# Performance work log

Measured on AMD Instinct MI355X. Metric: run time of the kernel, lower is better.

The kernel has to match this reference:

```python
import jax, jax.numpy as jnp
import numpy as np
import math

B, HW, C, HEADS = 32, 784, 384, 8
T = HW + 1            # 785 tokens incl. cls
TP = HW // 4 + 1      # 197 tokens after pooling
FF = 4 * C
EPS = 1e-5


def _ln2d(x, w, b):
    # nn.LayerNorm over last two dims (tokens, channels) with affine params
    mu = x.mean(axis=(-2, -1), keepdims=True)
    var = x.var(axis=(-2, -1), keepdims=True)
    return (x - mu) / jnp.sqrt(var + EPS) * w + b


def setup_inputs() -> dict:
    key = jax.random.key(0)
    ks = jax.random.split(key, 10)
    sc = math.sqrt(2.0 / C)  # kaiming-ish scale
    rn = lambda k, sh, s=1.0: (jax.random.normal(k, sh, jnp.float32) * s)
    return {
        "x": rn(ks[0], (B, HW, C)),
        "cls_token": rn(ks[1], (B, 1, C)),
        "w_ln1": jnp.ones((T, C), jnp.float32),
        "b_ln1": jnp.zeros((T, C), jnp.float32),
        "Wq": rn(ks[2], (C, C), sc),
        "Wk": rn(ks[3], (C, C), sc),
        "Wv": rn(ks[4], (C, C), sc),
        "Wo": rn(ks[5], (C, C), sc),
        "w_ln2": jnp.ones((TP, C), jnp.float32),
        "b_ln2": jnp.zeros((TP, C), jnp.float32),
        "W1": rn(ks[6], (FF, C), sc),
        "W2": rn(ks[7], (C, FF), math.sqrt(2.0 / FF)),
    }


def reference(x, cls_token, w_ln1, b_ln1, Wq, Wk, Wv, Wo, w_ln2, b_ln2, W1, W2):
    d = C // HEADS
    x_in = jnp.concatenate([cls_token, x], axis=1)           # (B,T,C)
    x1 = _ln2d(x_in, w_ln1, b_ln1)
    # MHSA (dropout disabled for determinism)
    q = (x1 @ Wq.T).reshape(B, T, HEADS, d)
    k = (x1 @ Wk.T).reshape(B, T, HEADS, d)
    v = (x1 @ Wv.T).reshape(B, T, HEADS, d)
    attn = jax.nn.softmax(jnp.einsum('bqhd,bkhd->bhqk', q, k) / math.sqrt(d), axis=-1)
    x_mhsa = jnp.einsum('bhqk,bkhd->bqhd', attn, v).reshape(B, T, C) @ Wo.T
    x_res1 = x_in + x_mhsa
    # Pooling block: channel importance from mean-pooled edge aggregation
    nodes = x_res1[:, 1:]                                     # (B,HW,C)
    ci = jax.nn.sigmoid(x_mhsa.mean(axis=1))                  # (B,C)  AvgPool1d(kernel=T)
    ca = jnp.einsum('bnc,bc->bn', nodes, ci)                  # (B,HW) channel aggregation
    idx = jnp.argsort(ca, axis=1)                             # ascending, like torch.sort
    nodes_sorted = jnp.take_along_axis(nodes, idx[:, :, None], axis=1)
    nodes_pooled = nodes_sorted[:, (HW // 4) * 3:]            # keep top quarter (largest ca)
    x2 = jnp.concatenate([x_res1[:, 0:1], nodes_pooled], axis=1)  # (B,TP,C)
    x2n = _ln2d(x2, w_ln2, b_ln2)
    # MLP (exact-erf GELU, as F.gelu default)
    h = jax.nn.gelu(x2n @ W1.T, approximate=False) @ W2.T
    x_res2 = x2n + h
    return x_res2[:, 1:], x_res2[:, 0:1]
```

## Files before the change

kernel.cpp:

```cpp
#include <hip/hip_runtime.h>
#include <hip/hip_bf16.h>
#include <math.h>

typedef __hip_bfloat16 bf16;
typedef _Float16 f16;
typedef __attribute__((ext_vector_type(8))) _Float16 f16x8;
typedef __attribute__((ext_vector_type(4))) _Float16 f16x4;
typedef __attribute__((ext_vector_type(4))) float f32x4;

#define B_ 32
#define HW_ 784
#define T_ 785
#define TP_ 197
#define C_ 384
#define H_ 8
#define D_ 48
#define FF_ 1536

#define MFMA16(a, b, c) __builtin_amdgcn_mfma_f32_16x16x32_f16(a, b, c, 0, 0, 0)

static constexpr size_t NRES = (size_t)B_ * T_ * C_;
static constexpr size_t NX   = (size_t)B_ * HW_ * C_;
static constexpr size_t NCLS = (size_t)B_ * C_;
static constexpr size_t NLN1 = (size_t)T_ * C_;
static constexpr size_t NWP  = (size_t)C_ * C_;
static constexpr size_t NLN2 = (size_t)TP_ * C_;
static constexpr size_t NW1  = (size_t)FF_ * C_;
static constexpr size_t NX2  = (size_t)B_ * TP_ * C_;
static constexpr size_t NH   = (size_t)B_ * TP_ * FF_;

static constexpr size_t NX1F = (size_t)1576 * 12 * 512;
static constexpr size_t NQKF = (size_t)256 * 56 * 2 * 512;
static constexpr size_t NVF  = (size_t)256 * 3 * 25 * 512;
static constexpr size_t NX2F = (size_t)400 * 12 * 512;
static constexpr size_t NHF  = (size_t)400 * 48 * 512;

static constexpr size_t XF_OFF   = 0;
static constexpr size_t CLSF_OFF = XF_OFF   + NX   * 4;
static constexpr size_t LN1W_OFF = CLSF_OFF + NCLS * 4;
static constexpr size_t LN1B_OFF = LN1W_OFF + NLN1 * 4;
static constexpr size_t WQF_OFF  = LN1B_OFF + NLN1 * 4;
static constexpr size_t LN2W_OFF = WQF_OFF  + 4 * NWP * 4;
static constexpr size_t LN2B_OFF = LN2W_OFF + NLN2 * 4;
static constexpr size_t W1F_OFF  = LN2B_OFF + NLN2 * 4;
static constexpr size_t W2F_OFF  = W1F_OFF  + NW1  * 4;
static constexpr size_t X1H_OFF  = W2F_OFF  + NW1  * 4;
static constexpr size_t X1L_OFF  = X1H_OFF  + NX1F * 2;
static constexpr size_t QFH_OFF  = X1L_OFF  + NX1F * 2;
static constexpr size_t QFL_OFF  = QFH_OFF  + NQKF * 2;
static constexpr size_t KFH_OFF  = QFL_OFF  + NQKF * 2;
static constexpr size_t KFL_OFF  = KFH_OFF  + NQKF * 2;
static constexpr size_t VFH_OFF  = KFL_OFF  + NQKF * 2;
static constexpr size_t VFL_OFF  = VFH_OFF  + NVF  * 2;
static constexpr size_t ATH_OFF  = VFL_OFF  + NVF  * 2;
static constexpr size_t ATL_OFF  = ATH_OFF  + NX1F * 2;
static constexpr size_t XM_OFF   = ATL_OFF  + NX1F * 2;
static constexpr size_t RES_OFF  = XM_OFF   + NRES * 4;
static constexpr size_t X2N_OFF  = RES_OFF  + NRES * 4;
static constexpr size_t X2NH_OFF = X2N_OFF  + NX2  * 4;
static constexpr size_t X2NL_OFF = X2NH_OFF + NX2F * 2;
static constexpr size_t HFH_OFF  = X2NL_OFF + NX2F * 2;
static constexpr size_t HFL_OFF  = HFH_OFF  + NHF  * 2;
static constexpr size_t WPH_OFF  = HFL_OFF  + NHF  * 2;
static constexpr size_t WPL_OFF  = WPH_OFF  + 4 * NWP * 2;
static constexpr size_t WFH_OFF  = WPL_OFF  + 4 * NWP * 2;
static constexpr size_t WFL_OFF  = WFH_OFF  + 2 * NW1 * 2;
static constexpr size_t MU_OFF   = WFL_OFF  + 2 * NW1 * 2;
static constexpr size_t RS_OFF   = MU_OFF   + 128;
static constexpr size_t CID_OFF  = RS_OFF   + 128;
static constexpr size_t CAD_OFF  = CID_OFF  + NCLS * 8;
static constexpr size_t PERM_OFF = CAD_OFF  + (size_t)B_ * HW_ * 8;
static constexpr size_t FLAG_OFF = PERM_OFF + (size_t)B_ * (TP_ - 1) * 4;
static constexpr size_t PS_OFF   = FLAG_OFF + 16;
static constexpr size_t CIP_OFF  = PS_OFF + 32 * 16 * 16;
static constexpr size_t L2PS_OFF = CIP_OFF + (size_t)B_ * 8 * C_ * 8;
static constexpr size_t L2MU_OFF = L2PS_OFF + 32 * 8 * 16;
static constexpr size_t L2RS_OFF = L2MU_OFF + 128;
static constexpr size_t PART_OFF = L2RS_OFF + 128;
static constexpr size_t ARENA_BYTES = PART_OFF + 2 * NX2 * 4;

__device__ __align__(256) unsigned char g_arena[ARENA_BYTES];

template <typename Tp>
__device__ __forceinline__ Tp* ap(size_t off) { return (Tp*)(g_arena + off); }

__device__ __forceinline__ void splitf(float v, f16& h, f16& l)
{
    float a = fabsf(v);
    f16 hv = (a >= 6.103515625e-05f) ? (f16)v : (f16)0.f;
    h = hv;
    l = (f16)((v - (float)hv) * 4096.f);
}

__device__ __forceinline__ size_t afrag(int row, int c, int KC)
{
    return ((size_t)((row >> 4) * KC + (c >> 5)) << 9)
         + (size_t)(((row & 15) | (((c >> 3) & 3) << 4)) << 3) + (c & 7);
}

__global__ void detect_kernel(const unsigned* __restrict__ w)
{
    if (threadIdx.x == 0)
        *ap<int>(FLAG_OFF) = (w[0] == 0x3F803F80u) ? 1 : 0;
}

struct SrcPtrs { const void* p[12]; };
static constexpr size_t SEGB[13] = {
    0,
    NX,
    NX + NCLS,
    NX + NCLS + NLN1,
    NX + NCLS + 2 * NLN1,
    NX + NCLS + 2 * NLN1 + NWP,
    NX + NCLS + 2 * NLN1 + 2 * NWP,
    NX + NCLS + 2 * NLN1 + 3 * NWP,
    NX + NCLS + 2 * NLN1 + 4 * NWP,
    NX + NCLS + 2 * NLN1 + 4 * NWP + NLN2,
    NX + NCLS + 2 * NLN1 + 4 * NWP + 2 * NLN2,
    NX + NCLS + 2 * NLN1 + 4 * NWP + 2 * NLN2 + NW1,
    NX + NCLS + 2 * NLN1 + 4 * NWP + 2 * NLN2 + 2 * NW1,
};
static constexpr size_t NTOT_CVT = SEGB[12];

__global__ __launch_bounds__(256) void cvt_all_kernel(SrcPtrs sp)
{
    size_t i = (size_t)blockIdx.x * 256 + threadIdx.x;
    if (i >= NTOT_CVT) return;
    int seg = 0;
#pragma unroll
    for (int k = 1; k < 12; k++) seg += (i >= SEGB[k]);
    size_t li = i - SEGB[seg];
    const void* src = sp.p[seg];
    float v = (*ap<int>(FLAG_OFF))
        ? __bfloat162float(((const bf16*)src)[li])
        : ((const float*)src)[li];
    ap<float>(XF_OFF)[i] = v;
}

__global__ __launch_bounds__(256) void wrepack_kernel()
{
    size_t i = (size_t)blockIdx.x * 256 + threadIdx.x;
    const size_t n1 = 4 * NWP;
    if (i >= n1 + 2 * NW1) return;
    float v; f16 *oh, *ol;
    if (i < n1) {
        size_t u = i;
        int blk = (int)(u >> 9), le = (int)(u & 511);
        int l = le >> 3, e = le & 7;
        int nt = blk / 12, kc = blk - nt * 12;
        int n = nt * 16 + (l & 15), k = kc * 32 + ((l >> 4) << 3) + e;
        v = ap<float>(WQF_OFF)[(size_t)n * C_ + k];
        oh = ap<f16>(WPH_OFF) + i; ol = ap<f16>(WPL_OFF) + i;
    } else if (i < n1 + NW1) {
        size_t u = i - n1;
        int blk = (int)(u >> 9), le = (int)(u & 511);
        int l = le >> 3, e = le & 7;
        int nt = blk / 12, kc = blk - nt * 12;
        int n = nt * 16 + (l & 15), k = kc * 32 + ((l >> 4) << 3) + e;
        v = ap<float>(W1F_OFF)[(size_t)n * C_ + k];
        oh = ap<f16>(WFH_OFF) + u; ol = ap<f16>(WFL_OFF) + u;
    } else {
        size_t u = i - n1 - NW1;
        int blk = (int)(u >> 9), le = (int)(u & 511);
        int l = le >> 3, e = le & 7;
        int nt = blk / 48, kc = blk - nt * 48;
        int n = nt * 16 + (l & 15), k = kc * 32 + ((l >> 4) << 3) + e;
        v = ap<float>(W2F_OFF)[(size_t)n * FF_ + k];
        oh = ap<f16>(WFH_OFF) + NW1 + u; ol = ap<f16>(WFL_OFF) + NW1 + u;
    }
    f16 h, lo; splitf(v, h, lo);
    *oh = h; *ol = lo;
}

__device__ __forceinline__ float xin_val(int b, int t, int c)
{
    return (t == 0) ? ap<float>(CLSF_OFF)[b * C_ + c]
                    : ap<float>(XF_OFF)[((size_t)b * HW_ + (t - 1)) * C_ + c];
}

__global__ __launch_bounds__(256) void stats1a_kernel()
{
    const int TC = T_ * C_;
    const int SL = (TC + 15) / 16;
    int b = blockIdx.x, s = blockIdx.y, tid = threadIdx.x;
    int e0 = s * SL, e1 = min(e0 + SL, TC);
    __shared__ double r1[256], r2[256];
    double sm = 0.0, s2 = 0.0;
    for (int e = e0 + tid; e < e1; e += 256) {
        int t = e / C_, c = e - t * C_;
        double v = (double)xin_val(b, t, c);
        sm += v; s2 += v * v;
    }
    r1[tid] = sm; r2[tid] = s2; __syncthreads();
    for (int o = 128; o; o >>= 1) {
        if (tid < o) { r1[tid] += r1[tid + o]; r2[tid] += r2[tid + o]; }
        __syncthreads();
    }
    if (tid == 0) {
        double2* ps = ap<double2>(PS_OFF);
        ps[b * 16 + s] = make_double2(r1[0], r2[0]);
    }
}

__global__ __launch_bounds__(64) void stats1b_kernel()
{
    int b = blockIdx.x, lane = threadIdx.x;
    const double2* ps = ap<double2>(PS_OFF);
    double sm = 0.0, s2 = 0.0;
    if (lane < 16) { sm = ps[b * 16 + lane].x; s2 = ps[b * 16 + lane].y; }
    for (int o = 8; o; o >>= 1) { sm += __shfl_down(sm, o); s2 += __shfl_down(s2, o); }
    if (lane == 0) {
        const int TC = T_ * C_;
        double m = sm / TC;
        double var = s2 / TC - m * m;
        ap<float>(MU_OFF)[b] = (float)m;
        ap<float>(RS_OFF)[b] = (float)(1.0 / sqrt(var + 1e-5));
    }
}

__global__ __launch_bounds__(256) void ln1_apply_kernel()
{
    size_t i = (size_t)blockIdx.x * 256 + threadIdx.x;
    if (i >= NRES) return;
    int grow = (int)(i / C_);
    int c = (int)(i - (size_t)grow * C_);
    int b = grow / T_, t = grow - b * T_;
    float v = xin_val(b, t, c);
    float r = (v - ap<float>(MU_OFF)[b]) * ap<float>(RS_OFF)[b]
              * ap<float>(LN1W_OFF)[t * C_ + c]
              + ap<float>(LN1B_OFF)[t * C_ + c];
    f16 h, l; splitf(r, h, l);
    size_t off = afrag(grow, c, 12);
    ap<f16>(X1H_OFF)[off] = h;
    ap<f16>(X1L_OFF)[off] = l;
}

template<int EMODE>
__global__ __launch_bounds__(256, 2) void gemm_fd(
    size_t ah_off, size_t al_off, size_t bh_off, size_t bl_off,
    size_t c_off, int M, int N, int KC, int GY)
{
    int nwg = (int)gridDim.x;
    int lin = blockIdx.x;
    int q8 = nwg >> 3, r8 = nwg & 7, xcd = lin & 7, pos = lin >> 3;
    int wg = (xcd < r8 ? xcd * (q8 + 1) : r8 * (q8 + 1) + (xcd - r8) * q8) + pos;
    int bx = wg / GY, by = wg - bx * GY;
    int kbeg = 0, kend = KC;
    if (EMODE == 6) { int ks = KC >> 1; kbeg = blockIdx.z * ks; kend = kbeg + ks; }
    int tid = threadIdx.x, w = tid >> 6, l = tid & 63;
    int wmt = bx * 8 + (w >> 1) * 4;
    int wnt = by * 8 + (w & 1) * 4;
    const f16* gAh = ap<f16>(ah_off);
    const f16* gAl = ap<f16>(al_off);
    const f16* gBh = ap<f16>(bh_off);
    const f16* gBl = ap<f16>(bl_off);
    size_t ab = (size_t)wmt * KC * 512 + (size_t)l * 8;
    size_t bb = (size_t)wnt * KC * 512 + (size_t)l * 8;

    const f32x4 zf = {0.f, 0.f, 0.f, 0.f};
    f32x4 acc1[4][4], acc2[4][4];
#pragma unroll
    for (int i = 0; i < 4; i++)
#pragma unroll
        for (int j = 0; j < 4; j++) { acc1[i][j] = zf; acc2[i][j] = zf; }

    for (int kc = kbeg; kc < kend; kc++) {
        f16x8 fah[4], fal[4], fbh[4], fbl[4];
#pragma unroll
        for (int i = 0; i < 4; i++) {
            size_t ao = ab + (size_t)(i * KC + kc) * 512;
            size_t bo = bb + (size_t)(i * KC + kc) * 512;
            fah[i] = *(const f16x8*)(gAh + ao);
            fal[i] = *(const f16x8*)(gAl + ao);
            fbh[i] = *(const f16x8*)(gBh + bo);
            fbl[i] = *(const f16x8*)(gBl + bo);
        }
        __builtin_amdgcn_s_setprio(1);
#pragma unroll
        for (int i = 0; i < 4; i++)
#pragma unroll
            for (int j = 0; j < 4; j++) {
                acc1[i][j] = MFMA16(fah[i], fbh[j], acc1[i][j]);
                acc2[i][j] = MFMA16(fah[i], fbl[j], acc2[i][j]);
                acc2[i][j] = MFMA16(fal[i], fbh[j], acc2[i][j]);
            }
        __builtin_amdgcn_s_setprio(0);
    }

    int l4 = ((l >> 4) << 2), lr = l & 15;
#pragma unroll
    for (int i = 0; i < 4; i++) {
        int rowb = (wmt + i) * 16 + l4;
#pragma unroll
        for (int j = 0; j < 4; j++) {
            int col = (wnt + j) * 16 + lr;
#pragma unroll
            for (int r = 0; r < 4; r++) {
                int row = rowb + r;
                if (row >= M) continue;
                float v = acc1[i][j][r] + acc2[i][j][r] * 0.000244140625f;
                if (EMODE == 5) {
                    int seg = col / C_;
                    int cn = col - seg * C_;
                    int hh = cn / D_, dd = cn - hh * D_;
                    int b2 = row / T_, t2 = row - b2 * T_;
                    int bh = b2 * H_ + hh;
                    f16 h, lo; splitf(v, h, lo);
                    if (seg < 2) {
                        size_t off = ((size_t)(bh * 112 + (t2 >> 4) * 2 + (dd >> 5)) << 9)
                                   + (size_t)(((t2 & 15) | (((dd >> 3) & 3) << 4)) << 3) + (dd & 7);
                        if (seg == 0) { ap<f16>(QFH_OFF)[off] = h; ap<f16>(QFL_OFF)[off] = lo; }
                        else          { ap<f16>(KFH_OFF)[off] = h; ap<f16>(KFL_OFF)[off] = lo; }
                    } else {
                        size_t off = ((size_t)(bh * 75 + (dd >> 4) * 25 + (t2 >> 5)) << 9)
                                   + (size_t)(((dd & 15) | (((t2 >> 3) & 3) << 4)) << 3) + (t2 & 7);
                        ap<f16>(VFH_OFF)[off] = h; ap<f16>(VFL_OFF)[off] = lo;
                    }
                } else if (EMODE == 4) {
                    ap<float>(c_off)[(size_t)row * N + col] = v;
                    int b2 = row / T_, t2 = row - b2 * T_;
                    ap<float>(RES_OFF)[(size_t)row * N + col] = v + xin_val(b2, t2, col);
                } else if (EMODE == 2) {
                    float g = 0.5f * v * (1.f + erff(v * 0.70710678f));
                    f16 h, lo; splitf(g, h, lo);
                    size_t off = afrag(row, col, 48);
                    ap<f16>(HFH_OFF)[off] = h;
                    ap<f16>(HFL_OFF)[off] = lo;
                } else {
                    ap<float>(PART_OFF)[(size_t)blockIdx.z * NX2 + (size_t)row * N + col] = v;
                }
            }
        }
    }
}

__global__ __launch_bounds__(256) void flash_kernel()
{
    __shared__ f16 Plds[4][2][16][40];
    int bh = blockIdx.y;
    int wv = threadIdx.x >> 6, l = threadIdx.x & 63;
    int qt = blockIdx.x * 4 + wv;
    if (qt >= 50) return;
    int b = bh >> 3, h = bh & 7;
    size_t qkb = (size_t)bh * 57344;
    const f16* QH = ap<f16>(QFH_OFF) + qkb;
    const f16* QL = ap<f16>(QFL_OFF) + qkb;
    const f16* KH = ap<f16>(KFH_OFF) + qkb;
    const f16* KL = ap<f16>(KFL_OFF) + qkb;
    const f16* VH = ap<f16>(VFH_OFF) + (size_t)bh * 38400;
    const f16* VL = ap<f16>(VFL_OFF) + (size_t)bh * 38400;
    int myq = l & 15, g = l >> 4;

    f16x8 qh[2], ql[2];
#pragma unroll
    for (int kc = 0; kc < 2; kc++) {
        size_t qo = ((size_t)(qt * 2 + kc) << 9) + (size_t)l * 8;
        qh[kc] = *(const f16x8*)(QH + qo);
        ql[kc] = *(const f16x8*)(QL + qo);
    }
    const f32x4 zf = {0.f, 0.f, 0.f, 0.f};
    f32x4 o1[3] = {zf, zf, zf}, o2[3] = {zf, zf, zf};
    float mrun = -3e38f, srun = 0.f;
    const float scale = 0.14433756729740643f;

    for (int w = 0; w < 25; w++) {
        f32x4 s1[2] = {zf, zf}, s2[2] = {zf, zf};
#pragma unroll
        for (int kt2 = 0; kt2 < 2; kt2++) {
            int kt = w * 2 + kt2;
#pragma unroll
            for (int kc = 0; kc < 2; kc++) {
                size_t ko = ((size_t)(kt * 2 + kc) << 9) + (size_t)l * 8;
                f16x8 kh = *(const f16x8*)(KH + ko);
                f16x8 kl = *(const f16x8*)(KL + ko);
                s1[kt2] = MFMA16(kh, qh[kc], s1[kt2]);
                s2[kt2] = MFMA16(kh, ql[kc], s2[kt2]);
                s2[kt2] = MFMA16(kl, qh[kc], s2[kt2]);
            }
        }
        float sv[8];
#pragma unroll
        for (int kt2 = 0; kt2 < 2; kt2++)
#pragma unroll
            for (int r = 0; r < 4; r++)
                sv[kt2 * 4 + r] = (s1[kt2][r] + s2[kt2][r] * 0.000244140625f) * scale;
        if (w == 24) {
#pragma unroll
            for (int kt2 = 0; kt2 < 2; kt2++)
#pragma unroll
                for (int r = 0; r < 4; r++)
                    if (kt2 * 16 + g * 4 + r >= 17) sv[kt2 * 4 + r] = -1e30f;
        }
        float pm = sv[0];
#pragma unroll
        for (int j2 = 1; j2 < 8; j2++) pm = fmaxf(pm, sv[j2]);
        pm = fmaxf(pm, __shfl_xor(pm, 16));
        pm = fmaxf(pm, __shfl_xor(pm, 32));
        float mnew = fmaxf(mrun, pm);
        float fac = __expf(mrun - mnew);
        mrun = mnew;
        float pv[8]; float ls = 0.f;
#pragma unroll
        for (int j2 = 0; j2 < 8; j2++) { pv[j2] = __expf(sv[j2] - mnew); ls += pv[j2]; }
        ls += __shfl_xor(ls, 16);
        ls += __shfl_xor(ls, 32);
        srun = srun * fac + ls;
        float fr[4];
#pragma unroll
        for (int r = 0; r < 4; r++) fr[r] = __shfl(fac, g * 4 + r);
#pragma unroll
        for (int j = 0; j < 3; j++)
#pragma unroll
            for (int r = 0; r < 4; r++) { o1[j][r] *= fr[r]; o2[j][r] *= fr[r]; }
#pragma unroll
        for (int kt2 = 0; kt2 < 2; kt2++) {
            f16x4 hh, llo;
#pragma unroll
            for (int r = 0; r < 4; r++) { f16 a, bb2; splitf(pv[kt2 * 4 + r], a, bb2); hh[r] = a; llo[r] = bb2; }
            *(f16x4*)&Plds[wv][0][myq][kt2 * 16 + g * 4] = hh;
            *(f16x4*)&Plds[wv][1][myq][kt2 * 16 + g * 4] = llo;
        }
        f16x8 pah = *(const f16x8*)&Plds[wv][0][myq][g * 8];
        f16x8 pal = *(const f16x8*)&Plds[wv][1][myq][g * 8];
#pragma unroll
        for (int j = 0; j < 3; j++) {
            size_t vo = ((size_t)(j * 25 + w) << 9) + (size_t)l * 8;
            f16x8 vh = *(const f16x8*)(VH + vo);
            f16x8 vl = *(const f16x8*)(VL + vo);
            o1[j] = MFMA16(pah, vh, o1[j]);
            o2[j] = MFMA16(pah, vl, o2[j]);
            o2[j] = MFMA16(pal, vh, o2[j]);
        }
    }
    float inv = 1.f / srun;
    float ir[4];
#pragma unroll
    for (int r = 0; r < 4; r++) ir[r] = __shfl(inv, g * 4 + r);
#pragma unroll
    for (int j = 0; j < 3; j++) {
        int c = h * D_ + j * 16 + myq;
#pragma unroll
        for (int r = 0; r < 4; r++) {
            int q = qt * 16 + g * 4 + r;
            if (q >= T_) continue;
            float v = (o1[j][r] + o2[j][r] * 0.000244140625f) * ir[r];
            int grow = b * T_ + q;
            f16 hv, lv; splitf(v, hv, lv);
            size_t off = afrag(grow, c, 12);
            ap<f16>(ATH_OFF)[off] = hv;
            ap<f16>(ATL_OFF)[off] = lv;
        }
    }
}

__global__ __launch_bounds__(384) void cia_kernel()
{
    int b = blockIdx.x, s = blockIdx.y, c = threadIdx.x;
    const float* xm = ap<float>(XM_OFF);
    const int SL = (T_ + 7) / 8;
    int t0 = s * SL, t1 = min(t0 + SL, T_);
    double sm = 0.0;
    for (int t = t0; t < t1; t++) sm += (double)xm[((size_t)b * T_ + t) * C_ + c];
    ap<double>(CIP_OFF)[((size_t)b * 8 + s) * C_ + c] = sm;
}

__global__ __launch_bounds__(384) void cib_kernel()
{
    int b = blockIdx.x, c = threadIdx.x;
    const double* pp = ap<double>(CIP_OFF);
    double sm = 0.0;
#pragma unroll
    for (int s = 0; s < 8; s++) sm += pp[((size_t)b * 8 + s) * C_ + c];
    sm /= (double)T_;
    ap<double>(CID_OFF)[b * C_ + c] = 1.0 / (1.0 + exp(-sm));
}

__global__ __launch_bounds__(64) void ca_kernel()
{
    const float* xres1 = ap<float>(RES_OFF);
    const double* ci   = ap<double>(CID_OFF);
    int idx = blockIdx.x;
    int b = idx / HW_, n = idx - b * HW_;
    int lane = threadIdx.x;
    double s = 0.0;
    for (int c = lane; c < C_; c += 64)
        s += (double)xres1[((size_t)b * T_ + 1 + n) * C_ + c] * ci[b * C_ + c];
    for (int o = 32; o; o >>= 1) s += __shfl_down(s, o);
    if (lane == 0) ap<double>(CAD_OFF)[idx] = s;
}

__global__ __launch_bounds__(256) void rank_kernel()
{
    const double* ca = ap<double>(CAD_OFF);
    int* perm = ap<int>(PERM_OFF);
    int b = blockIdx.x, tid = threadIdx.x;
    __shared__ double cs[HW_];
    for (int i = tid; i < HW_; i += 256) cs[i] = ca[b * HW_ + i];
    __syncthreads();
    for (int i = tid; i < HW_; i += 256) {
        double vi = cs[i];
        int r = 0;
        for (int j = 0; j < HW_; j++) {
            double vj = cs[j];
            r += (vj < vi) || (vj == vi && j < i);
        }
        if (r >= HW_ - TP_ + 1) perm[b * (TP_ - 1) + (r - (HW_ - TP_ + 1))] = i;
    }
}

__global__ __launch_bounds__(256) void ln2a_kernel()
{
    const float* xres1 = ap<float>(RES_OFF);
    const int* perm = ap<int>(PERM_OFF);
    const int TC = TP_ * C_;
    const int SL = (TC + 7) / 8;
    int b = blockIdx.x, s = blockIdx.y, tid = threadIdx.x;
    int e0 = s * SL, e1 = min(e0 + SL, TC);
    __shared__ double r1[256], r2[256];
    double sm = 0.0, s2 = 0.0;
    for (int e = e0 + tid; e < e1; e += 256) {
        int t = e / C_, c = e - t * C_;
        int st = (t == 0) ? 0 : 1 + perm[b * (TP_ - 1) + t - 1];
        double v = (double)xres1[((size_t)b * T_ + st) * C_ + c];
        sm += v; s2 += v * v;
    }
    r1[tid] = sm; r2[tid] = s2; __syncthreads();
    for (int o = 128; o; o >>= 1) {
        if (tid < o) { r1[tid] += r1[tid + o]; r2[tid] += r2[tid + o]; }
        __syncthreads();
    }
    if (tid == 0) {
        double2* ps = ap<double2>(L2PS_OFF);
        ps[b * 8 + s] = make_double2(r1[0], r2[0]);
    }
}

__global__ __launch_bounds__(64) void ln2b_kernel()
{
    int b = blockIdx.x, lane = threadIdx.x;
    const double2* ps = ap<double2>(L2PS_OFF);
    double sm = 0.0, s2 = 0.0;
    if (lane < 8) { sm = ps[b * 8 + lane].x; s2 = ps[b * 8 + lane].y; }
    for (int o = 4; o; o >>= 1) { sm += __shfl_down(sm, o); s2 += __shfl_down(s2, o); }
    if (lane == 0) {
        const int TC = TP_ * C_;
        double m = sm / TC;
        double var = s2 / TC - m * m;
        ap<float>(L2MU_OFF)[b] = (float)m;
        ap<float>(L2RS_OFF)[b] = (float)(1.0 / sqrt(var + 1e-5));
    }
}

__global__ __launch_bounds__(256) void ln2_apply_kernel()
{
    size_t i = (size_t)blockIdx.x * 256 + threadIdx.x;
    if (i >= NX2) return;
    const int TC = TP_ * C_;
    int b = (int)(i / TC);
    int e = (int)(i - (size_t)b * TC);
    int t = e / C_, c = e - t * C_;
    const int* perm = ap<int>(PERM_OFF);
    int st = (t == 0) ? 0 : 1 + perm[b * (TP_ - 1) + t - 1];
    float v = ap<float>(RES_OFF)[((size_t)b * T_ + st) * C_ + c];
    float r = (v - ap<float>(L2MU_OFF)[b]) * ap<float>(L2RS_OFF)[b]
              * ap<float>(LN2W_OFF)[e] + ap<float>(LN2B_OFF)[e];
    ap<float>(X2N_OFF)[i] = r;
    int grow = b * TP_ + t;
    f16 h, l; splitf(r, h, l);
    size_t off = afrag(grow, c, 12);
    ap<f16>(X2NH_OFF)[off] = h;
    ap<f16>(X2NL_OFF)[off] = l;
}

__global__ __launch_bounds__(256) void ffn2_reduce_kernel(float* __restrict__ out)
{
    const size_t tot = NX2;
    size_t i = (size_t)blockIdx.x * 256 + threadIdx.x;
    if (i >= tot) return;
    const float* part = ap<float>(PART_OFF);
    float v = part[i] + part[tot + i] + ap<float>(X2N_OFF)[i];
    int gm = (int)(i / C_);
    int gn = (int)(i - (size_t)gm * C_);
    int b = gm / TP_, t = gm - b * TP_;
    size_t off = (t == 0)
        ? ((size_t)B_ * (TP_ - 1) * C_ + (size_t)b * C_ + gn)
        : ((size_t)(b * (TP_ - 1) + (t - 1)) * C_ + gn);
    out[off] = v;
}

extern "C" void kernel_launch(void* const* d_in, const int* in_sizes, int n_in,
                              void* d_out, int out_size, void* d_ws, size_t ws_size,
                              hipStream_t stream)
{
    float* out = (float*)d_out;
    (void)d_ws; (void)ws_size; (void)in_sizes; (void)n_in; (void)out_size;

    const int M1 = B_ * T_;
    const int M2 = B_ * TP_;

    detect_kernel<<<1, 64, 0, stream>>>((const unsigned*)d_in[2]);
    SrcPtrs sp;
    for (int i = 0; i < 12; i++) sp.p[i] = d_in[i];
    cvt_all_kernel<<<(int)((NTOT_CVT + 255) / 256), 256, 0, stream>>>(sp);
    wrepack_kernel<<<(int)((4 * NWP + 2 * NW1 + 255) / 256), 256, 0, stream>>>();

    stats1a_kernel<<<dim3(B_, 16), 256, 0, stream>>>();
    stats1b_kernel<<<B_, 64, 0, stream>>>();
    ln1_apply_kernel<<<(int)((NRES + 255) / 256), 256, 0, stream>>>();

    gemm_fd<5><<<dim3(197 * 9), 256, 0, stream>>>(
        X1H_OFF, X1L_OFF, WPH_OFF, WPL_OFF, 0, M1, 3 * C_, 12, 9);

    flash_kernel<<<dim3(13, 256), 256, 0, stream>>>();

    gemm_fd<4><<<dim3(197 * 3), 256, 0, stream>>>(
        ATH_OFF, ATL_OFF,
        WPH_OFF + (size_t)442368 * 2, WPL_OFF + (size_t)442368 * 2,
        XM_OFF, M1, C_, 12, 3);

    cia_kernel<<<dim3(B_, 8), 384, 0, stream>>>();
    cib_kernel<<<B_, 384, 0, stream>>>();
    ca_kernel<<<B_ * HW_, 64, 0, stream>>>();
    rank_kernel<<<B_, 256, 0, stream>>>();
    ln2a_kernel<<<dim3(B_, 8), 256, 0, stream>>>();
    ln2b_kernel<<<B_, 64, 0, stream>>>();
    ln2_apply_kernel<<<(int)((NX2 + 255) / 256), 256, 0, stream>>>();

    gemm_fd<2><<<dim3(50 * 12), 256, 0, stream>>>(
        X2NH_OFF, X2NL_OFF, WFH_OFF, WFL_OFF, 0, M2, FF_, 12, 12);
    gemm_fd<6><<<dim3(50 * 3, 1, 2), 256, 0, stream>>>(
        HFH_OFF, HFL_OFF, WFH_OFF + NW1 * 2, WFL_OFF + NW1 * 2, 0, M2, C_, 48, 3);
    ffn2_reduce_kernel<<<(int)((NX2 + 255) / 256), 256, 0, stream>>>(out);
}
```

Before: 1.057 ms.

## Process two query tiles per wave in flash attention to reuse K/V loads

Each wave now handles two 16-row query tiles, so every K and V fragment loaded from global memory feeds twice the MFMA work, which halves K/V traffic per query. The softmax scale is folded into Q in the QKV GEMM epilogue, the O rescale is skipped when the running max does not change, and the grid is flattened with an XCD-aware remap so the blocks of one head share an L2. The cost is more registers per wave and fewer waves in total, which may lower occupancy and latency hiding.

```diff
diff --git a/kernel.cpp b/kernel.cpp
--- a/kernel.cpp
+++ b/kernel.cpp
@@ -305,7 +305,8 @@
                     int hh = cn / D_, dd = cn - hh * D_;
                     int b2 = row / T_, t2 = row - b2 * T_;
                     int bh = b2 * H_ + hh;
-                    f16 h, lo; splitf(v, h, lo);
+                    float vv = (seg == 0) ? v * 0.14433756729740643f : v;
+                    f16 h, lo; splitf(vv, h, lo);
                     if (seg < 2) {
                         size_t off = ((size_t)(bh * 112 + (t2 >> 4) * 2 + (dd >> 5)) << 9)
                                    + (size_t)(((t2 & 15) | (((dd >> 3) & 3) << 4)) << 3) + (dd & 7);
@@ -336,11 +337,15 @@
 
 __global__ __launch_bounds__(256) void flash_kernel()
 {
-    __shared__ f16 Plds[4][2][16][40];
-    int bh = blockIdx.y;
+    __shared__ f16 Plds[4][2][2][16][40];
+    int nwg = (int)gridDim.x;
+    int lin = blockIdx.x;
+    int q8 = nwg >> 3, r8 = nwg & 7, xcd = lin & 7, pos = lin >> 3;
+    int wg = (xcd < r8 ? xcd * (q8 + 1) : r8 * (q8 + 1) + (xcd - r8) * q8) + pos;
+    int bh = wg / 7, qblk = wg - bh * 7;
     int wv = threadIdx.x >> 6, l = threadIdx.x & 63;
-    int qt = blockIdx.x * 4 + wv;
-    if (qt >= 50) return;
+    int qt0 = qblk * 8 + wv * 2;
+    if (qt0 >= 50) return;
     int b = bh >> 3, h = bh & 7;
     size_t qkb = (size_t)bh * 57344;
     const f16* QH = ap<f16>(QFH_OFF) + qkb;
@@ -351,104 +356,127 @@
     const f16* VL = ap<f16>(VFL_OFF) + (size_t)bh * 38400;
     int myq = l & 15, g = l >> 4;
 
-    f16x8 qh[2], ql[2];
-#pragma unroll
-    for (int kc = 0; kc < 2; kc++) {
-        size_t qo = ((size_t)(qt * 2 + kc) << 9) + (size_t)l * 8;
-        qh[kc] = *(const f16x8*)(QH + qo);
-        ql[kc] = *(const f16x8*)(QL + qo);
-    }
+    f16x8 qh[2][2], ql[2][2];
+#pragma unroll
+    for (int u = 0; u < 2; u++)
+#pragma unroll
+        for (int kc = 0; kc < 2; kc++) {
+            size_t qo = ((size_t)((qt0 + u) * 2 + kc) << 9) + (size_t)l * 8;
+            qh[u][kc] = *(const f16x8*)(QH + qo);
+            ql[u][kc] = *(const f16x8*)(QL + qo);
+        }
     const f32x4 zf = {0.f, 0.f, 0.f, 0.f};
-    f32x4 o1[3] = {zf, zf, zf}, o2[3] = {zf, zf, zf};
-    float mrun = -3e38f, srun = 0.f;
-    const float scale = 0.14433756729740643f;
+    f32x4 o1[2][3], o2[2][3];
+#pragma unroll
+    for (int u = 0; u < 2; u++)
+#pragma unroll
+        for (int j = 0; j < 3; j++) { o1[u][j] = zf; o2[u][j] = zf; }
+    float mrun[2] = {-3e38f, -3e38f}, srun[2] = {0.f, 0.f};
 
     for (int w = 0; w < 25; w++) {
-        f32x4 s1[2] = {zf, zf}, s2[2] = {zf, zf};
-#pragma unroll
-        for (int kt2 = 0; kt2 < 2; kt2++) {
-            int kt = w * 2 + kt2;
+        f16x8 kh[2][2], kl[2][2];
+#pragma unroll
+        for (int kt2 = 0; kt2 < 2; kt2++)
 #pragma unroll
             for (int kc = 0; kc < 2; kc++) {
-                size_t ko = ((size_t)(kt * 2 + kc) << 9) + (size_t)l * 8;
-                f16x8 kh = *(const f16x8*)(KH + ko);
-                f16x8 kl = *(const f16x8*)(KL + ko);
-                s1[kt2] = MFMA16(kh, qh[kc], s1[kt2]);
-                s2[kt2] = MFMA16(kh, ql[kc], s2[kt2]);
-                s2[kt2] = MFMA16(kl, qh[kc], s2[kt2]);
-            }
-        }
-        float sv[8];
-#pragma unroll
-        for (int kt2 = 0; kt2 < 2; kt2++)
-#pragma unroll
-            for (int r = 0; r < 4; r++)
-                sv[kt2 * 4 + r] = (s1[kt2][r] + s2[kt2][r] * 0.000244140625f) * scale;
-        if (w == 24) {
-#pragma unroll
-            for (int kt2 = 0; kt2 < 2; kt2++)
-#pragma unroll
-                for (int r = 0; r < 4; r++)
-                    if (kt2 * 16 + g * 4 + r >= 17) sv[kt2 * 4 + r] = -1e30f;
-        }
-        float pm = sv[0];
-#pragma unroll
-        for (int j2 = 1; j2 < 8; j2++) pm = fmaxf(pm, sv[j2]);
-        pm = fmaxf(pm, __shfl_xor(pm, 16));
-        pm = fmaxf(pm, __shfl_xor(pm, 32));
-        float mnew = fmaxf(mrun, pm);
-        float fac = __expf(mrun - mnew);
-        mrun = mnew;
-        float pv[8]; float ls = 0.f;
-#pragma unroll
-        for (int j2 = 0; j2 < 8; j2++) { pv[j2] = __expf(sv[j2] - mnew); ls += pv[j2]; }
-        ls += __shfl_xor(ls, 16);
-        ls += __shfl_xor(ls, 32);
-        srun = srun * fac + ls;
-        float fr[4];
-#pragma unroll
-        for (int r = 0; r < 4; r++) fr[r] = __shfl(fac, g * 4 + r);
-#pragma unroll
-        for (int j = 0; j < 3; j++)
-#pragma unroll
-            for (int r = 0; r < 4; r++) { o1[j][r] *= fr[r]; o2[j][r] *= fr[r]; }
-#pragma unroll
-        for (int kt2 = 0; kt2 < 2; kt2++) {
-            f16x4 hh, llo;
-#pragma unroll
-            for (int r = 0; r < 4; r++) { f16 a, bb2; splitf(pv[kt2 * 4 + r], a, bb2); hh[r] = a; llo[r] = bb2; }
-            *(f16x4*)&Plds[wv][0][myq][kt2 * 16 + g * 4] = hh;
-            *(f16x4*)&Plds[wv][1][myq][kt2 * 16 + g * 4] = llo;
-        }
-        f16x8 pah = *(const f16x8*)&Plds[wv][0][myq][g * 8];
-        f16x8 pal = *(const f16x8*)&Plds[wv][1][myq][g * 8];
+                size_t ko = ((size_t)((w * 2 + kt2) * 2 + kc) << 9) + (size_t)l * 8;
+                kh[kt2][kc] = *(const f16x8*)(KH + ko);
+                kl[kt2][kc] = *(const f16x8*)(KL + ko);
+            }
+        f16x8 vh[3], vl[3];
 #pragma unroll
         for (int j = 0; j < 3; j++) {
             size_t vo = ((size_t)(j * 25 + w) << 9) + (size_t)l * 8;
-            f16x8 vh = *(const f16x8*)(VH + vo);
-            f16x8 vl = *(const f16x8*)(VL + vo);
-            o1[j] = MFMA16(pah, vh, o1[j]);
-            o2[j] = MFMA16(pah, vl, o2[j]);
-            o2[j] = MFMA16(pal, vh, o2[j]);
+            vh[j] = *(const f16x8*)(VH + vo);
+            vl[j] = *(const f16x8*)(VL + vo);
         }
-    }
-    float inv = 1.f / srun;
-    float ir[4];
-#pragma unroll
-    for (int r = 0; r < 4; r++) ir[r] = __shfl(inv, g * 4 + r);
-#pragma unroll
-    for (int j = 0; j < 3; j++) {
-        int c = h * D_ + j * 16 + myq;
-#pragma unroll
-        for (int r = 0; r < 4; r++) {
-            int q = qt * 16 + g * 4 + r;
-            if (q >= T_) continue;
-            float v = (o1[j][r] + o2[j][r] * 0.000244140625f) * ir[r];
-            int grow = b * T_ + q;
-            f16 hv, lv; splitf(v, hv, lv);
-            size_t off = afrag(grow, c, 12);
-            ap<f16>(ATH_OFF)[off] = hv;
-            ap<f16>(ATL_OFF)[off] = lv;
+#pragma unroll
+        for (int u = 0; u < 2; u++) {
+            f32x4 s1[2] = {zf, zf}, s2[2] = {zf, zf};
+#pragma unroll
+            for (int kt2 = 0; kt2 < 2; kt2++)
+#pragma unroll
+                for (int kc = 0; kc < 2; kc++) {
+                    s1[kt2] = MFMA16(kh[kt2][kc], qh[u][kc], s1[kt2]);
+                    s2[kt2] = MFMA16(kh[kt2][kc], ql[u][kc], s2[kt2]);
+                    s2[kt2] = MFMA16(kl[kt2][kc], qh[u][kc], s2[kt2]);
+                }
+            float sv[8];
+#pragma unroll
+            for (int kt2 = 0; kt2 < 2; kt2++)
+#pragma unroll
+                for (int r = 0; r < 4; r++)
+                    sv[kt2 * 4 + r] = s1[kt2][r] + s2[kt2][r] * 0.000244140625f;
+            if (w == 24) {
+#pragma unroll
+                for (int kt2 = 0; kt2 < 2; kt2++)
+#pragma unroll
+                    for (int r = 0; r < 4; r++)
+                        if (kt2 * 16 + g * 4 + r >= 17) sv[kt2 * 4 + r] = -1e30f;
+            }
+            float pm = sv[0];
+#pragma unroll
+            for (int j2 = 1; j2 < 8; j2++) pm = fmaxf(pm, sv[j2]);
+            pm = fmaxf(pm, __shfl_xor(pm, 16));
+            pm = fmaxf(pm, __shfl_xor(pm, 32));
+            float mnew = fmaxf(mrun[u], pm);
+            float pv[8]; float ls = 0.f;
+#pragma unroll
+            for (int j2 = 0; j2 < 8; j2++) { pv[j2] = __expf(sv[j2] - mnew); ls += pv[j2]; }
+            ls += __shfl_xor(ls, 16);
+            ls += __shfl_xor(ls, 32);
+            if (__any(pm > mrun[u])) {
+                float fac = __expf(mrun[u] - mnew);
+                float fr[4];
+#pragma unroll
+                for (int r = 0; r < 4; r++) fr[r] = __shfl(fac, g * 4 + r);
+#pragma unroll
+                for (int j = 0; j < 3; j++)
+#pragma unroll
+                    for (int r = 0; r < 4; r++) { o1[u][j][r] *= fr[r]; o2[u][j][r] *= fr[r]; }
+                srun[u] = srun[u] * fac + ls;
+                mrun[u] = mnew;
+            } else {
+                srun[u] += ls;
+            }
+#pragma unroll
+            for (int kt2 = 0; kt2 < 2; kt2++) {
+                f16x4 hh, llo;
+#pragma unroll
+                for (int r = 0; r < 4; r++) { f16 a, bb2; splitf(pv[kt2 * 4 + r], a, bb2); hh[r] = a; llo[r] = bb2; }
+                *(f16x4*)&Plds[wv][u][0][myq][kt2 * 16 + g * 4] = hh;
+                *(f16x4*)&Plds[wv][u][1][myq][kt2 * 16 + g * 4] = llo;
+            }
+            f16x8 pah = *(const f16x8*)&Plds[wv][u][0][myq][g * 8];
+            f16x8 pal = *(const f16x8*)&Plds[wv][u][1][myq][g * 8];
+#pragma unroll
+            for (int j = 0; j < 3; j++) {
+                o1[u][j] = MFMA16(pah, vh[j], o1[u][j]);
+                o2[u][j] = MFMA16(pah, vl[j], o2[u][j]);
+                o2[u][j] = MFMA16(pal, vh[j], o2[u][j]);
+            }
+        }
+    }
+#pragma unroll
+    for (int u = 0; u < 2; u++) {
+        float inv = 1.f / srun[u];
+        float ir[4];
+#pragma unroll
+        for (int r = 0; r < 4; r++) ir[r] = __shfl(inv, g * 4 + r);
+#pragma unroll
+        for (int j = 0; j < 3; j++) {
+            int c = h * D_ + j * 16 + myq;
+#pragma unroll
+            for (int r = 0; r < 4; r++) {
+                int q = (qt0 + u) * 16 + g * 4 + r;
+                if (q >= T_) continue;
+                float v = (o1[u][j][r] + o2[u][j][r] * 0.000244140625f) * ir[r];
+                int grow = b * T_ + q;
+                f16 hv, lv; splitf(v, hv, lv);
+                size_t off = afrag(grow, c, 12);
+                ap<f16>(ATH_OFF)[off] = hv;
+                ap<f16>(ATL_OFF)[off] = lv;
+            }
         }
     }
 }
@@ -611,7 +639,7 @@
     gemm_fd<5><<<dim3(197 * 9), 256, 0, stream>>>(
         X1H_OFF, X1L_OFF, WPH_OFF, WPL_OFF, 0, M1, 3 * C_, 12, 9);
 
-    flash_kernel<<<dim3(13, 256), 256, 0, stream>>>();
+    flash_kernel<<<dim3(256 * 7), 256, 0, stream>>>();
 
     gemm_fd<4><<<dim3(197 * 3), 256, 0, stream>>>(
         ATH_OFF, ATL_OFF,
```

New measurement: 912.8 us. 1.16x faster.
